# Performance work log

Measured on AMD Instinct MI355X. Metric: run time of the kernel, lower is better.

The kernel has to match this reference:

```python
import jax, jax.numpy as jnp
import numpy as np

T = 128        # number of timesteps (init arg T)
LEN_M = 32     # causal window length (init arg len_M)
N = 8192       # nodes
F = 64         # features per node


def setup_inputs() -> dict:
    key = jax.random.key(0)
    k1, k2, k3 = jax.random.split(key, 3)
    X = jax.random.normal(k1, (T, N, F), dtype=jnp.float32)
    # M_pad[r] holds the length-(r+1) parameter M[str(r+1)] in its first r+1 slots
    # (padding is masked out before softmax, so its values are irrelevant).
    M_pad = jax.random.normal(k2, (LEN_M, LEN_M), dtype=jnp.float32)
    # M_big[j] corresponds to parameter key str(LEN_M+1+j); keys LEN_M+1..T-1 are
    # used by rows LEN_M+1..T-1 (row LEN_M reuses M[str(LEN_M)] = M_pad[-1], per the source).
    M_big = jax.random.normal(k3, (T - LEN_M - 1, LEN_M), dtype=jnp.float32)
    return {"X": X, "M_pad": M_pad, "M_big": M_big}


def _band_weights(M_pad, M_big):
    """Build the [T, T] causal banded mixing matrix with per-row softmax weights."""
    cols = jnp.arange(LEN_M)
    # rows 0..LEN_M-1: softmax over the growing prefix window of length row+1
    prefix_mask = cols[None, :] <= jnp.arange(LEN_M)[:, None]            # [LEN_M, LEN_M]
    w_small = jax.nn.softmax(jnp.where(prefix_mask, M_pad, -jnp.inf), axis=1)
    # rows LEN_M..T-1 use key str(row): row==LEN_M reuses M_pad[-1], rest use M_big
    logits_big = jnp.concatenate([M_pad[LEN_M - 1:LEN_M], M_big], axis=0)  # [T-LEN_M, LEN_M]
    w_big = jax.nn.softmax(logits_big, axis=1)
    W = jnp.zeros((T, T), dtype=M_pad.dtype)
    W = W.at[:LEN_M, :LEN_M].set(w_small)  # w_small is zero outside the prefix window
    rows = jnp.arange(LEN_M, T)
    cidx = (rows - LEN_M + 1)[:, None] + cols[None, :]  # sliding window cols per row
    W = W.at[rows[:, None], cidx].set(w_big)
    return W


def reference(X, M_pad, M_big):
    W = _band_weights(M_pad, M_big)          # [T, T] banded
    data = X.reshape(T, -1)                  # [T, N*F]
    out = W @ data                           # causal windowed weighted sum, all rows at once
    return out.reshape(X.shape)
```

## Files before the change

### kernel.cpp

```cpp
#include <hip/hip_runtime.h>
#include <math.h>

#define T_     128
#define LENM   32
#define NCOL   (8192 * 64)
#define WSLOTS 48
#define GRP    8

typedef float f4_t __attribute__((ext_vector_type(4)));

__global__ void build_w_kernel(const float* __restrict__ M_pad,
                               const float* __restrict__ M_big,
                               float* __restrict__ Wc) {
    int t = threadIdx.x;
    if (t >= T_) return;
    const float* src;
    int len, joff;
    if (t < LENM)       { src = M_pad + t * LENM;              len = t + 1; joff = LENM - 1 - t; }
    else if (t == LENM) { src = M_pad + (LENM - 1) * LENM;     len = LENM;  joff = 0; }
    else                { src = M_big + (t - LENM - 1) * LENM; len = LENM;  joff = 0; }

    float m = -3.4e38f;
    for (int j = 0; j < len; ++j) m = fmaxf(m, src[j]);
    float e[LENM];
    float s = 0.f;
    for (int j = 0; j < len; ++j) { e[j] = expf(src[j] - m); s += e[j]; }
    float inv = 1.f / s;
    for (int j = 0; j < LENM; ++j) Wc[t * LENM + j] = 0.f;
    for (int j = 0; j < len; ++j)  Wc[t * LENM + joff + j] = e[j] * inv;
}


template<int ROW>
__device__ __forceinline__ void load_row(const f4_t* __restrict__ xp,
                                         f4_t (&WIN)[WSLOTS]) {
    WIN[ROW % WSLOTS] = xp[(size_t)ROW * (NCOL / 4)];
}

template<int R0, int CNT>
__device__ __forceinline__ void load_rows(const f4_t* __restrict__ xp,
                                          f4_t (&WIN)[WSLOTS]) {
    if constexpr (CNT > 0) {
        load_row<R0>(xp, WIN);
        load_rows<R0 + 1, CNT - 1>(xp, WIN);
    }
}

template<int ROW>
__device__ __forceinline__ void compute_row(f4_t* __restrict__ op,
                                            const f4_t* w4,
                                            const f4_t (&WIN)[WSLOTS]) {
    constexpr int jmin_ = (ROW < LENM) ? (LENM - 1 - ROW) : 0;
    f4_t acc; acc.x = 0.f; acc.y = 0.f; acc.z = 0.f; acc.w = 0.f;
#pragma unroll
    for (int q = 0; q < 8; ++q) {
        if (q * 4 + 3 >= jmin_) {
            f4_t w = w4[ROW * 8 + q];
#pragma unroll
            for (int m = 0; m < 4; ++m) {
                const int j = q * 4 + m;
                if (j >= jmin_) {
                    f4_t xv = WIN[(ROW - (LENM - 1) + j) % WSLOTS];
                    float wm = (m == 0) ? w.x : (m == 1) ? w.y
                             : (m == 2) ? w.z : w.w;
                    acc.x = fmaf(wm, xv.x, acc.x);
                    acc.y = fmaf(wm, xv.y, acc.y);
                    acc.z = fmaf(wm, xv.z, acc.z);
                    acc.w = fmaf(wm, xv.w, acc.w);
                }
            }
        }
    }
    __builtin_nontemporal_store(acc, &op[(size_t)ROW * (NCOL / 4)]);
}

template<int R0, int CNT>
__device__ __forceinline__ void compute_rows(f4_t* __restrict__ op,
                                             const f4_t* w4,
                                             const f4_t (&WIN)[WSLOTS]) {
    if constexpr (CNT > 0) {
        compute_row<R0>(op, w4, WIN);
        compute_rows<R0 + 1, CNT - 1>(op, w4, WIN);
    }
}

template<int G>
__device__ __forceinline__ void do_group(const f4_t* __restrict__ xp,
                                         f4_t* __restrict__ op,
                                         const f4_t* w4,
                                         f4_t (&WIN)[WSLOTS]) {
    if constexpr (G * GRP + GRP < T_)
        load_rows<G * GRP + GRP, GRP>(xp, WIN);
    __builtin_amdgcn_sched_barrier(0);
    compute_rows<G * GRP, GRP>(op, w4, WIN);
}

template<int G>
__device__ __forceinline__ void run_groups(const f4_t* __restrict__ xp,
                                           f4_t* __restrict__ op,
                                           const f4_t* w4,
                                           f4_t (&WIN)[WSLOTS]) {
    if constexpr (G * GRP < T_) {
        do_group<G>(xp, op, w4, WIN);
        run_groups<G + 1>(xp, op, w4, WIN);
    }
}

__global__ __launch_bounds__(256, 2) void band_mix_kernel(
    const float* __restrict__ X,
    const float* __restrict__ Wc,
    float* __restrict__ out) {
    __shared__ f4_t w4[T_ * LENM / 4];
    for (int i = threadIdx.x; i < T_ * LENM / 4; i += 256)
        w4[i] = reinterpret_cast<const f4_t*>(Wc)[i];
    __syncthreads();

    const int c = (blockIdx.x * 256 + threadIdx.x) * 4;
    const f4_t* xp = reinterpret_cast<const f4_t*>(X + c);
    f4_t* op = reinterpret_cast<f4_t*>(out + c);

    f4_t WIN[WSLOTS];
    load_rows<0, GRP>(xp, WIN);

    run_groups<0>(xp, op, w4, WIN);
}

extern "C" void kernel_launch(void* const* d_in, const int* in_sizes, int n_in,
                              void* d_out, int out_size, void* d_ws, size_t ws_size,
                              hipStream_t stream) {
    const float* X     = (const float*)d_in[0];
    const float* M_pad = (const float*)d_in[1];
    const float* M_big = (const float*)d_in[2];
    float* out = (float*)d_out;
    float* Wc  = (float*)d_ws;

    build_w_kernel<<<1, 128, 0, stream>>>(M_pad, M_big, Wc);
    band_mix_kernel<<<NCOL / 4 / 256, 256, 0, stream>>>(X, Wc, out);
}
```

Measured before the change: 106.6 us.

## Stream X rows through double-buffered LDS via global_load_lds DMA

Replaces direct per-thread global loads of X rows into a register window with asynchronous global_load_lds transfers into two LDS buffers of eight rows each. Each group waits on vmcnt, copies its rows from LDS into a smaller register window, starts the DMA for the next group, then computes. This is meant to cut register pressure and overlap loading with computation. In exchange it adds about 64KB of LDS per block, which may limit occupancy. The vmcnt wait also counts outstanding stores, so it may stall more than needed.

```diff
diff --git a/kernel.cpp b/kernel.cpp
--- a/kernel.cpp
+++ b/kernel.cpp
@@ -4,8 +4,9 @@
 #define T_     128
 #define LENM   32
 #define NCOL   (8192 * 64)
-#define WSLOTS 48
+#define WSLOTS 40
 #define GRP    8
+#define NGRP   (T_ / GRP)
 
 typedef float f4_t __attribute__((ext_vector_type(4)));
 
@@ -32,24 +33,42 @@
 
 
 template<int ROW>
-__device__ __forceinline__ void load_row(const f4_t* __restrict__ xp,
-                                         f4_t (&WIN)[WSLOTS]) {
-    WIN[ROW % WSLOTS] = xp[(size_t)ROW * (NCOL / 4)];
+__device__ __forceinline__ void dma_row(const float* __restrict__ xg,
+                                        f4_t (&buf)[GRP * 256], int tid) {
+    __builtin_amdgcn_global_load_lds(
+        (const __attribute__((address_space(1))) void*)(xg + (size_t)ROW * NCOL),
+        (__attribute__((address_space(3))) void*)&buf[(ROW % GRP) * 256 + tid],
+        16, 0, 0);
 }
 
 template<int R0, int CNT>
-__device__ __forceinline__ void load_rows(const f4_t* __restrict__ xp,
-                                          f4_t (&WIN)[WSLOTS]) {
+__device__ __forceinline__ void dma_rows(const float* __restrict__ xg,
+                                         f4_t (&buf)[GRP * 256], int tid) {
     if constexpr (CNT > 0) {
-        load_row<R0>(xp, WIN);
-        load_rows<R0 + 1, CNT - 1>(xp, WIN);
+        dma_row<R0>(xg, buf, tid);
+        dma_rows<R0 + 1, CNT - 1>(xg, buf, tid);
     }
 }
 
 template<int ROW>
-__device__ __forceinline__ void compute_row(f4_t* __restrict__ op,
-                                            const f4_t* w4,
-                                            const f4_t (&WIN)[WSLOTS]) {
+__device__ __forceinline__ void pull_row(const f4_t (&buf)[GRP * 256], int tid,
+                                         f4_t (&W)[WSLOTS]) {
+    W[ROW % WSLOTS] = buf[(ROW % GRP) * 256 + tid];
+}
+
+template<int R0, int CNT>
+__device__ __forceinline__ void pull_rows(const f4_t (&buf)[GRP * 256], int tid,
+                                          f4_t (&W)[WSLOTS]) {
+    if constexpr (CNT > 0) {
+        pull_row<R0>(buf, tid, W);
+        pull_rows<R0 + 1, CNT - 1>(buf, tid, W);
+    }
+}
+
+template<int ROW>
+__device__ __forceinline__ void comp_row(f4_t* __restrict__ op,
+                                         const f4_t* w4,
+                                         const f4_t (&W)[WSLOTS]) {
     constexpr int jmin_ = (ROW < LENM) ? (LENM - 1 - ROW) : 0;
     f4_t acc; acc.x = 0.f; acc.y = 0.f; acc.z = 0.f; acc.w = 0.f;
 #pragma unroll
@@ -60,7 +79,7 @@
             for (int m = 0; m < 4; ++m) {
                 const int j = q * 4 + m;
                 if (j >= jmin_) {
-                    f4_t xv = WIN[(ROW - (LENM - 1) + j) % WSLOTS];
+                    f4_t xv = W[(ROW - (LENM - 1) + j + 2 * WSLOTS) % WSLOTS];
                     float wm = (m == 0) ? w.x : (m == 1) ? w.y
                              : (m == 2) ? w.z : w.w;
                     acc.x = fmaf(wm, xv.x, acc.x);
@@ -75,34 +94,46 @@
 }
 
 template<int R0, int CNT>
-__device__ __forceinline__ void compute_rows(f4_t* __restrict__ op,
-                                             const f4_t* w4,
-                                             const f4_t (&WIN)[WSLOTS]) {
+__device__ __forceinline__ void comp_rows(f4_t* __restrict__ op,
+                                          const f4_t* w4,
+                                          const f4_t (&W)[WSLOTS]) {
     if constexpr (CNT > 0) {
-        compute_row<R0>(op, w4, WIN);
-        compute_rows<R0 + 1, CNT - 1>(op, w4, WIN);
+        comp_row<R0>(op, w4, W);
+        comp_rows<R0 + 1, CNT - 1>(op, w4, W);
     }
 }
 
 template<int G>
-__device__ __forceinline__ void do_group(const f4_t* __restrict__ xp,
-                                         f4_t* __restrict__ op,
-                                         const f4_t* w4,
-                                         f4_t (&WIN)[WSLOTS]) {
-    if constexpr (G * GRP + GRP < T_)
-        load_rows<G * GRP + GRP, GRP>(xp, WIN);
+__device__ __forceinline__ void run_group(const float* __restrict__ xg,
+                                          f4_t* __restrict__ op,
+                                          const f4_t* w4,
+                                          f4_t (&bufA)[GRP * 256],
+                                          f4_t (&bufB)[GRP * 256],
+                                          int tid, f4_t (&W)[WSLOTS]) {
+    if constexpr (G == 0) asm volatile("s_waitcnt vmcnt(0)" ::: "memory");
+    else                  asm volatile("s_waitcnt vmcnt(8)" ::: "memory");
     __builtin_amdgcn_sched_barrier(0);
-    compute_rows<G * GRP, GRP>(op, w4, WIN);
+    if constexpr (G & 1) pull_rows<G * GRP, GRP>(bufB, tid, W);
+    else                 pull_rows<G * GRP, GRP>(bufA, tid, W);
+    __builtin_amdgcn_sched_barrier(0);
+    if constexpr (G + 1 < NGRP) {
+        if constexpr ((G + 1) & 1) dma_rows<(G + 1) * GRP, GRP>(xg, bufB, tid);
+        else                       dma_rows<(G + 1) * GRP, GRP>(xg, bufA, tid);
+    }
+    __builtin_amdgcn_sched_barrier(0);
+    comp_rows<G * GRP, GRP>(op, w4, W);
 }
 
 template<int G>
-__device__ __forceinline__ void run_groups(const f4_t* __restrict__ xp,
+__device__ __forceinline__ void run_groups(const float* __restrict__ xg,
                                            f4_t* __restrict__ op,
                                            const f4_t* w4,
-                                           f4_t (&WIN)[WSLOTS]) {
-    if constexpr (G * GRP < T_) {
-        do_group<G>(xp, op, w4, WIN);
-        run_groups<G + 1>(xp, op, w4, WIN);
+                                           f4_t (&bufA)[GRP * 256],
+                                           f4_t (&bufB)[GRP * 256],
+                                           int tid, f4_t (&W)[WSLOTS]) {
+    if constexpr (G < NGRP) {
+        run_group<G>(xg, op, w4, bufA, bufB, tid, W);
+        run_groups<G + 1>(xg, op, w4, bufA, bufB, tid, W);
     }
 }
 
@@ -111,18 +142,20 @@
     const float* __restrict__ Wc,
     float* __restrict__ out) {
     __shared__ f4_t w4[T_ * LENM / 4];
+    __shared__ f4_t bufA[GRP * 256];
+    __shared__ f4_t bufB[GRP * 256];
     for (int i = threadIdx.x; i < T_ * LENM / 4; i += 256)
         w4[i] = reinterpret_cast<const f4_t*>(Wc)[i];
     __syncthreads();
 
-    const int c = (blockIdx.x * 256 + threadIdx.x) * 4;
-    const f4_t* xp = reinterpret_cast<const f4_t*>(X + c);
+    const int tid = threadIdx.x;
+    const int c = (blockIdx.x * 256 + tid) * 4;
+    const float* xg = X + c;
     f4_t* op = reinterpret_cast<f4_t*>(out + c);
 
-    f4_t WIN[WSLOTS];
-    load_rows<0, GRP>(xp, WIN);
-
-    run_groups<0>(xp, op, w4, WIN);
+    f4_t W[WSLOTS];
+    dma_rows<0, GRP>(xg, bufA, tid);
+    run_groups<0>(xg, op, w4, bufA, bufB, tid, W);
 }
 
 extern "C" void kernel_launch(void* const* d_in, const int* in_sizes, int n_in,
```

Measured after the change: 102.7 us. 3.7% less time.
